# Kernel tuning notes

Hardware: AMD Instinct MI355X
Metric: run time of the kernel (lower is better)

Reference implementation:

```python
import jax, jax.numpy as jnp
import numpy as np

N, M = 100000, 800000
F_IN, F_E, H = 64, 16, 64
T_NODE, T_EDGE = 2, 3
HEAD_DIM = 16.0


def setup_inputs() -> dict:
    key = jax.random.key(0)
    ks = jax.random.split(key, 16)
    inp = {
        "x": jax.random.normal(ks[0], (N, F_IN), jnp.float32),
        "edge_feat": jax.random.normal(ks[1], (M, F_E), jnp.float32),
        "node_type": jax.random.randint(ks[2], (N,), 0, T_NODE, jnp.int32),
        "edge_src": jax.random.randint(ks[3], (M,), 0, N, jnp.int32),
        "edge_dst": jax.random.randint(ks[4], (M,), 0, N, jnp.int32),
        "edge_type": jax.random.randint(ks[5], (M,), 0, T_EDGE, jnp.int32),
    }
    s_n = 1.0 / np.sqrt(F_IN)
    s_e = 1.0 / np.sqrt(F_E)
    for i, name in enumerate(["W1", "W2", "W3", "W4"]):
        inp[name] = jax.random.normal(ks[6 + i], (T_NODE, F_IN, H), jnp.float32) * s_n
        inp["b" + name[1]] = jax.random.normal(ks[10 + i], (T_NODE, H), jnp.float32) * 0.01
    inp["W5"] = jax.random.normal(ks[14], (T_EDGE, F_E, H), jnp.float32) * s_e
    inp["b5"] = jax.random.normal(ks[15], (T_EDGE, H), jnp.float32) * 0.01
    return inp


def _node_proj(x, W, b, node_type):
    # per-node-type linear: [T,F,H] weights, select row per node type
    p = jnp.einsum('nf,tfh->tnh', x, W) + b[:, None, :]      # [T,N,H]
    return jnp.take_along_axis(p, node_type[None, :, None], axis=0)[0]  # [N,H]


def reference(x, edge_feat, W1, b1, W2, b2, W3, b3, W4, b4, W5, b5,
              node_type, edge_src, edge_dst, edge_type):
    n = x.shape[0]
    h1 = _node_proj(x, W1, b1, node_type)
    h2 = _node_proj(x, W2, b2, node_type)
    h3 = _node_proj(x, W3, b3, node_type)
    h4 = _node_proj(x, W4, b4, node_type)
    # per-edge-type linear via weight gather (F_E is small)
    w5e = jnp.einsum('mf,mfh->mh', edge_feat, W5[edge_type]) + b5[edge_type]  # [M,H]
    # scalar attention logit per edge (w3_i . (w4_j + w5_ij)) / sqrt(head_dim)
    num = jnp.sum(h3[edge_dst] * (h4[edge_src] + w5e), axis=-1)  # [M]
    # softmax over a single scalar per edge == 1.0 exactly (faithful to source)
    score = jax.nn.softmax((num / jnp.sqrt(HEAD_DIM))[:, None], axis=-1)[:, 0]  # [M]
    msg = score[:, None] * (h2[edge_src] + w5e)                  # [M,H]
    out = h1 + jax.ops.segment_sum(msg, edge_dst, num_segments=n)
    return out
```

## Files before the change

### kernel.cpp

```cpp
#include <hip/hip_runtime.h>


#define CAP 16
#define OVF_CAP 32768

typedef __attribute__((ext_vector_type(8))) short short8;
typedef __attribute__((ext_vector_type(4))) float f32x4;

__device__ __forceinline__ float b2f(unsigned short u) {
    union { unsigned v; float f; } x; x.v = ((unsigned)u) << 16; return x.f;
}
__device__ __forceinline__ unsigned short f2b(float f) {
    union { float f; unsigned v; } x; x.f = f;
    unsigned u = x.v;
    unsigned r = (u + 0x7FFFu + ((u >> 16) & 1u)) >> 16;
    return (unsigned short)r;
}

__global__ __launch_bounds__(256) void k1_gemm_scatter(
    const float* __restrict__ x, const int* __restrict__ nt,
    const float* __restrict__ W1, const float* __restrict__ b1,
    const float* __restrict__ W2, const float* __restrict__ b2,
    const int* __restrict__ esrc, const int* __restrict__ edst,
    const int* __restrict__ etype,
    int* __restrict__ cnt32, int* __restrict__ ovfCnt,
    int4* __restrict__ ovf, int2* __restrict__ rec,
    float* __restrict__ out, unsigned short* __restrict__ h2b,
    int N, int M)
{
    __shared__ __align__(16) unsigned short sx[128 * 72];
    __shared__ __align__(16) unsigned short sw[4][64 * 72];
    __shared__ int snt[128];

    int tid = threadIdx.x;

    if (blockIdx.x & 1) {
        int e0 = (blockIdx.x >> 1) * 1024 + tid;
        int dd[4], ssrc[4], tty[4];
        bool v[4];
#pragma unroll
        for (int j = 0; j < 4; ++j) {
            int e = e0 + j * 256;
            v[j] = e < M;
            int ec = v[j] ? e : 0;
            dd[j]   = edst[ec];
            ssrc[j] = esrc[ec];
            tty[j]  = etype[ec];
        }
        int pos[4];
#pragma unroll
        for (int j = 0; j < 4; ++j)
            if (v[j]) pos[j] = atomicAdd(&cnt32[dd[j]], 1);
#pragma unroll
        for (int j = 0; j < 4; ++j) {
            if (!v[j]) continue;
            int packed = ssrc[j] | (tty[j] << 20);
            int e = e0 + j * 256;
            if (pos[j] < CAP) {
                rec[dd[j] * CAP + pos[j]] = make_int2(packed, e);
            } else {
                int slot = atomicAdd(ovfCnt, 1);
                if (slot < OVF_CAP) ovf[slot] = make_int4(packed, e, dd[j], 0);
            }
        }
        return;
    }

    int rowbase = (blockIdx.x >> 1) * 128;

    const float* Wm0 = W1;
    const float* Wm1 = W1 + 4096;
    const float* Wm2 = W2;
    const float* Wm3 = W2 + 4096;
#pragma unroll
    for (int j = 0; j < 4; ++j) {
        int k  = (tid >> 4) + j * 16;
        int n4 = (tid & 15) * 4;
        float4 w0 = *(const float4*)&Wm0[k * 64 + n4];
        float4 w1v = *(const float4*)&Wm1[k * 64 + n4];
        float4 w2v = *(const float4*)&Wm2[k * 64 + n4];
        float4 w3 = *(const float4*)&Wm3[k * 64 + n4];
        sw[0][(n4 + 0) * 72 + k] = f2b(w0.x);
        sw[0][(n4 + 1) * 72 + k] = f2b(w0.y);
        sw[0][(n4 + 2) * 72 + k] = f2b(w0.z);
        sw[0][(n4 + 3) * 72 + k] = f2b(w0.w);
        sw[1][(n4 + 0) * 72 + k] = f2b(w1v.x);
        sw[1][(n4 + 1) * 72 + k] = f2b(w1v.y);
        sw[1][(n4 + 2) * 72 + k] = f2b(w1v.z);
        sw[1][(n4 + 3) * 72 + k] = f2b(w1v.w);
        sw[2][(n4 + 0) * 72 + k] = f2b(w2v.x);
        sw[2][(n4 + 1) * 72 + k] = f2b(w2v.y);
        sw[2][(n4 + 2) * 72 + k] = f2b(w2v.z);
        sw[2][(n4 + 3) * 72 + k] = f2b(w2v.w);
        sw[3][(n4 + 0) * 72 + k] = f2b(w3.x);
        sw[3][(n4 + 1) * 72 + k] = f2b(w3.y);
        sw[3][(n4 + 2) * 72 + k] = f2b(w3.z);
        sw[3][(n4 + 3) * 72 + k] = f2b(w3.w);
    }

    if (tid < 128) {
        int r = rowbase + tid;
        snt[tid] = (r < N) ? nt[r] : 0;
    }

    int fr = (tid & 15) * 4;
    int ir = tid >> 4;
#pragma unroll
    for (int it = 0; it < 8; ++it) {
        int i = it * 16 + ir;
        int r = rowbase + i;
        float4 v = make_float4(0.f, 0.f, 0.f, 0.f);
        if (r < N) v = *(const float4*)&x[(size_t)r * 64 + fr];
        ushort4 p;
        p.x = f2b(v.x); p.y = f2b(v.y); p.z = f2b(v.z); p.w = f2b(v.w);
        *(ushort4*)&sx[i * 72 + fr] = p;
    }
    __syncthreads();

    int lane = tid & 63;
    int wid  = tid >> 6;
    int q    = lane >> 4;
    int cc   = lane & 15;
    int m0   = wid * 32;

    f32x4 acc[4][2][4];
#pragma unroll
    for (int mm = 0; mm < 4; ++mm)
#pragma unroll
        for (int s = 0; s < 2; ++s)
#pragma unroll
            for (int t = 0; t < 4; ++t)
                acc[mm][s][t] = (f32x4){0.f, 0.f, 0.f, 0.f};

#pragma unroll
    for (int k0 = 0; k0 < 64; k0 += 32) {
        int ko = k0 + q * 8;
        short8 af0 = *(short8*)&sx[(m0 + cc) * 72 + ko];
        short8 af1 = *(short8*)&sx[(m0 + 16 + cc) * 72 + ko];
#pragma unroll
        for (int mm = 0; mm < 4; ++mm)
#pragma unroll
            for (int t = 0; t < 4; ++t) {
                short8 bf = *(short8*)&sw[mm][(t * 16 + cc) * 72 + ko];
                acc[mm][0][t] = __builtin_amdgcn_mfma_f32_16x16x32_bf16(
                    af0, bf, acc[mm][0][t], 0, 0, 0);
                acc[mm][1][t] = __builtin_amdgcn_mfma_f32_16x16x32_bf16(
                    af1, bf, acc[mm][1][t], 0, 0, 0);
            }
    }

    float b1v[2][4], b2v[2][4];
#pragma unroll
    for (int ty = 0; ty < 2; ++ty)
#pragma unroll
        for (int t = 0; t < 4; ++t) {
            b1v[ty][t] = b1[ty * 64 + t * 16 + cc];
            b2v[ty][t] = b2[ty * 64 + t * 16 + cc];
        }

#pragma unroll
    for (int s = 0; s < 2; ++s)
#pragma unroll
        for (int reg = 0; reg < 4; ++reg) {
            int rl = m0 + s * 16 + q * 4 + reg;
            int r = rowbase + rl;
            if (r < N) {
                int ty = snt[rl];
#pragma unroll
                for (int t = 0; t < 4; ++t) {
                    float v1 = (ty ? acc[1][s][t][reg] : acc[0][s][t][reg])
                               + b1v[ty][t];
                    float v2 = (ty ? acc[3][s][t][reg] : acc[2][s][t][reg])
                               + b2v[ty][t];
                    out[(size_t)r * 64 + t * 16 + cc] = v1;
                    h2b[(size_t)r * 64 + t * 16 + cc] = f2b(v2);
                }
            }
        }
}

__global__ __launch_bounds__(256) void k2_gather(
    const float* __restrict__ ef, const int2* __restrict__ rec,
    const int* __restrict__ cnt32,
    const float* __restrict__ W5, const float* __restrict__ b5,
    const int4* __restrict__ ovf, const int* __restrict__ ovfCnt,
    const unsigned short* __restrict__ h2b, float* __restrict__ out,
    int N, int gatherBlocks, int ovfBlocks)
{
    __shared__ float sW[3072 + 192];
    __shared__ float sG[4][64];

    int tid = threadIdx.x;
    for (int k = tid; k < 816; k += 256) {
        ((float4*)sW)[k] = (k < 768) ? ((const float4*)W5)[k]
                                     : ((const float4*)b5)[k - 768];
    }
    __syncthreads();

    int lane = tid & 63;
    int wid = tid >> 6;

    if (blockIdx.x >= (unsigned)gatherBlocks) {
        int novf = min(*ovfCnt, OVF_CAP);
        int gw = (blockIdx.x - gatherBlocks) * 4 + wid;
        int nw = ovfBlocks * 4;
        for (int ri = gw; ri < novf; ri += nw) {
            int4 o = ovf[ri];
            int s = o.x & 0xFFFFF;
            int t = (unsigned)o.x >> 20;
            float acc = sW[3072 + t * 64 + lane] +
                        b2f(h2b[(size_t)s * 64 + lane]);
#pragma unroll
            for (int f = 0; f < 16; ++f)
                acc = fmaf(ef[(size_t)o.y * 16 + f],
                           sW[(t * 16 + f) * 64 + lane], acc);
            unsafeAtomicAdd(&out[(size_t)o.z * 64 + lane], acc);
        }
        return;
    }

    int d = blockIdx.x * 4 + wid;
    bool active = d < N;
    int deg = 0;
    if (active) deg = min(cnt32[d], CAP);
    int base = d * CAP;

    int myt = (lane < 48) ? (lane >> 4) : (lane - 48);
    int myf = lane & 15;
    float accH = 0.f, accS = 0.f;

    for (int i = 0; i < deg; i += 8) {
        int nrem = deg - i;
        int2 r[8];
#pragma unroll
        for (int j = 0; j < 8; ++j) {
            int ij = i + j;
            ij = (ij < deg) ? ij : (deg - 1);
            r[j] = rec[base + ij];
        }
        float hv[8], ev[8];
#pragma unroll
        for (int j = 0; j < 8; ++j) {
            int s = r[j].x & 0xFFFFF;
            hv[j] = b2f(h2b[(size_t)s * 64 + lane]);
            ev[j] = ef[(size_t)r[j].y * 16 + myf];
        }
#pragma unroll
        for (int j = 0; j < 8; ++j) {
            int t = (unsigned)r[j].x >> 20;
            bool ok = j < nrem;
            accH += ok ? hv[j] : 0.f;
            float v = (lane < 48) ? ev[j] : 1.0f;
            accS += (ok && (t == myt)) ? v : 0.f;
        }
    }

    sG[wid][lane] = accS;
    float rr = accH;
    const float* g = sG[wid];
#pragma unroll
    for (int j = 0; j < 48; ++j)
        rr = fmaf(g[j], sW[j * 64 + lane], rr);
#pragma unroll
    for (int t = 0; t < 3; ++t)
        rr = fmaf(g[48 + t], sW[3072 + t * 64 + lane], rr);

    if (active)
        unsafeAtomicAdd(&out[(size_t)d * 64 + lane], rr);
}

extern "C" void kernel_launch(void* const* d_in, const int* in_sizes, int n_in,
                              void* d_out, int out_size, void* d_ws, size_t ws_size,
                              hipStream_t stream) {
    const float* x  = (const float*)d_in[0];
    const float* ef = (const float*)d_in[1];
    const int* nt   = (const int*)d_in[2];
    const int* es   = (const int*)d_in[3];
    const int* ed   = (const int*)d_in[4];
    const int* et   = (const int*)d_in[5];
    const float* W1 = (const float*)d_in[6];
    const float* b1 = (const float*)d_in[7];
    const float* W2 = (const float*)d_in[8];
    const float* b2 = (const float*)d_in[9];
    const float* W5 = (const float*)d_in[14];
    const float* b5 = (const float*)d_in[15];

    int N = in_sizes[2];
    int M = in_sizes[3];

    char* w = (char*)d_ws;
    size_t off = 0;
    unsigned short* h2b = (unsigned short*)(w + off); off += (size_t)N * 64 * 2;
    off = (off + 255) & ~(size_t)255;
    int2* rec = (int2*)(w + off); off += (size_t)N * CAP * 8;
    off = (off + 255) & ~(size_t)255;
    int4* ovf = (int4*)(w + off); off += (size_t)OVF_CAP * 16;
    off = (off + 255) & ~(size_t)255;
    int* ovfCnt = (int*)(w + off);
    int* cnt32  = (int*)(w + off + 64);
    size_t zeroBytes = 64 + (size_t)N * 4;

    float* out = (float*)d_out;

    hipMemsetAsync(ovfCnt, 0, zeroBytes, stream);

    int gemmBlocks    = (N + 127) / 128;
    int scatterBlocks = (M + 1023) / 1024;
    int gb1 = 2 * max(gemmBlocks, scatterBlocks);
    k1_gemm_scatter<<<gb1, 256, 0, stream>>>(
        x, nt, W1, b1, W2, b2, es, ed, et,
        cnt32, ovfCnt, ovf, rec, out, h2b, N, M);

    int gatherBlocks = (N + 3) / 4;
    int ovfBlocks = 32;
    k2_gather<<<gatherBlocks + ovfBlocks, 256, 0, stream>>>(
        ef, rec, cnt32, W5, b5, ovf, ovfCnt, h2b, out,
        N, gatherBlocks, ovfBlocks);
}
```

Measured before the change: 306.6 us.

## Replace capped per-node buckets with counting-sort binning by 32-node groups

```diff
diff --git a/kernel.cpp b/kernel.cpp
--- a/kernel.cpp
+++ b/kernel.cpp
@@ -1,8 +1,8 @@
 #include <hip/hip_runtime.h>
 
 
-#define CAP 16
-#define OVF_CAP 32768
+#define ABLK 64
+#define TS   3200
 
 typedef __attribute__((ext_vector_type(8))) short short8;
 typedef __attribute__((ext_vector_type(4))) float f32x4;
@@ -17,85 +17,121 @@
     return (unsigned short)r;
 }
 
-__global__ __launch_bounds__(256) void k1_gemm_scatter(
+__global__ __launch_bounds__(256) void k_hist(
+    const int* __restrict__ edst, int* __restrict__ table,
+    int M, int NB, int epb)
+{
+    __shared__ int h[TS];
+    int tid = threadIdx.x;
+    for (int t = tid; t < TS; t += 256) h[t] = 0;
+    __syncthreads();
+    int base = blockIdx.x * epb;
+    for (int i = tid; i < epb; i += 256) {
+        int e = base + i;
+        if (e < M) atomicAdd(&h[edst[e] >> 5], 1);
+    }
+    __syncthreads();
+    for (int t = tid; t < NB; t += 256) table[blockIdx.x * TS + t] = h[t];
+}
+
+__global__ __launch_bounds__(256) void k_colsum(
+    const int* __restrict__ table, int* __restrict__ totals, int NB)
+{
+    int t = blockIdx.x * 256 + threadIdx.x;
+    if (t >= NB) return;
+    int s = 0;
+    for (int j = 0; j < ABLK; ++j) s += table[j * TS + t];
+    totals[t] = s;
+}
+
+__global__ __launch_bounds__(256) void k_prefix(
+    const int* __restrict__ totals, int* __restrict__ starts, int NB, int M)
+{
+    __shared__ int ps[256];
+    int tid = threadIdx.x;
+    int per = (NB + 255) / 256;
+    int lo = tid * per, hi = min(lo + per, NB);
+    int s = 0;
+    for (int i = lo; i < hi; ++i) s += totals[i];
+    ps[tid] = s;
+    __syncthreads();
+    int run = s;
+    for (int off = 1; off < 256; off <<= 1) {
+        int tmp = (tid >= off) ? ps[tid - off] : 0;
+        __syncthreads();
+        run += tmp;
+        ps[tid] = run;
+        __syncthreads();
+    }
+    int r = run - s;
+    for (int i = lo; i < hi; ++i) { starts[i] = r; r += totals[i]; }
+    if (tid == 255) starts[NB] = M;
+}
+
+__global__ __launch_bounds__(256) void k_offsets(
+    int* __restrict__ table, const int* __restrict__ starts, int NB)
+{
+    int t = blockIdx.x * 256 + threadIdx.x;
+    if (t >= NB) return;
+    int run = starts[t];
+    for (int j = 0; j < ABLK; ++j) {
+        int v = table[j * TS + t];
+        table[j * TS + t] = run;
+        run += v;
+    }
+}
+
+__global__ __launch_bounds__(256) void k3_gemm_binscatter(
     const float* __restrict__ x, const int* __restrict__ nt,
     const float* __restrict__ W1, const float* __restrict__ b1,
     const float* __restrict__ W2, const float* __restrict__ b2,
     const int* __restrict__ esrc, const int* __restrict__ edst,
     const int* __restrict__ etype,
-    int* __restrict__ cnt32, int* __restrict__ ovfCnt,
-    int4* __restrict__ ovf, int2* __restrict__ rec,
+    const int* __restrict__ table, int2* __restrict__ rec,
     float* __restrict__ out, unsigned short* __restrict__ h2b,
-    int N, int M)
-{
-    __shared__ __align__(16) unsigned short sx[128 * 72];
-    __shared__ __align__(16) unsigned short sw[4][64 * 72];
-    __shared__ int snt[128];
+    int N, int M, int NB, int epb)
+{
+    __shared__ __align__(16) char smem[55808];
 
     int tid = threadIdx.x;
 
-    if (blockIdx.x & 1) {
-        int e0 = (blockIdx.x >> 1) * 1024 + tid;
-        int dd[4], ssrc[4], tty[4];
-        bool v[4];
-#pragma unroll
-        for (int j = 0; j < 4; ++j) {
-            int e = e0 + j * 256;
-            v[j] = e < M;
-            int ec = v[j] ? e : 0;
-            dd[j]   = edst[ec];
-            ssrc[j] = esrc[ec];
-            tty[j]  = etype[ec];
-        }
-        int pos[4];
-#pragma unroll
-        for (int j = 0; j < 4; ++j)
-            if (v[j]) pos[j] = atomicAdd(&cnt32[dd[j]], 1);
-#pragma unroll
-        for (int j = 0; j < 4; ++j) {
-            if (!v[j]) continue;
-            int packed = ssrc[j] | (tty[j] << 20);
-            int e = e0 + j * 256;
-            if (pos[j] < CAP) {
-                rec[dd[j] * CAP + pos[j]] = make_int2(packed, e);
-            } else {
-                int slot = atomicAdd(ovfCnt, 1);
-                if (slot < OVF_CAP) ovf[slot] = make_int4(packed, e, dd[j], 0);
-            }
+    if (blockIdx.x < ABLK) {
+        int* loc = (int*)smem;
+        int b = blockIdx.x;
+        for (int t = tid; t < NB; t += 256) loc[t] = table[b * TS + t];
+        __syncthreads();
+        int base = b * epb;
+        for (int i = tid; i < epb; i += 256) {
+            int e = base + i;
+            if (e >= M) break;
+            int d = edst[e];
+            int bkt = d >> 5, dloc = d & 31;
+            int pos = atomicAdd(&loc[bkt], 1);
+            int packed = esrc[e] | (etype[e] << 17) | (dloc << 19);
+            rec[pos] = make_int2(packed, e);
         }
         return;
     }
 
-    int rowbase = (blockIdx.x >> 1) * 128;
-
-    const float* Wm0 = W1;
-    const float* Wm1 = W1 + 4096;
-    const float* Wm2 = W2;
-    const float* Wm3 = W2 + 4096;
+    unsigned short* sx = (unsigned short*)smem;
+    unsigned short* sw = (unsigned short*)(smem + 18432);
+    int* snt = (int*)(smem + 55296);
+
+    int rowbase = (blockIdx.x - ABLK) * 128;
+
+    const float* Wm[4] = { W1, W1 + 4096, W2, W2 + 4096 };
 #pragma unroll
     for (int j = 0; j < 4; ++j) {
         int k  = (tid >> 4) + j * 16;
         int n4 = (tid & 15) * 4;
-        float4 w0 = *(const float4*)&Wm0[k * 64 + n4];
-        float4 w1v = *(const float4*)&Wm1[k * 64 + n4];
-        float4 w2v = *(const float4*)&Wm2[k * 64 + n4];
-        float4 w3 = *(const float4*)&Wm3[k * 64 + n4];
-        sw[0][(n4 + 0) * 72 + k] = f2b(w0.x);
-        sw[0][(n4 + 1) * 72 + k] = f2b(w0.y);
-        sw[0][(n4 + 2) * 72 + k] = f2b(w0.z);
-        sw[0][(n4 + 3) * 72 + k] = f2b(w0.w);
-        sw[1][(n4 + 0) * 72 + k] = f2b(w1v.x);
-        sw[1][(n4 + 1) * 72 + k] = f2b(w1v.y);
-        sw[1][(n4 + 2) * 72 + k] = f2b(w1v.z);
-        sw[1][(n4 + 3) * 72 + k] = f2b(w1v.w);
-        sw[2][(n4 + 0) * 72 + k] = f2b(w2v.x);
-        sw[2][(n4 + 1) * 72 + k] = f2b(w2v.y);
-        sw[2][(n4 + 2) * 72 + k] = f2b(w2v.z);
-        sw[2][(n4 + 3) * 72 + k] = f2b(w2v.w);
-        sw[3][(n4 + 0) * 72 + k] = f2b(w3.x);
-        sw[3][(n4 + 1) * 72 + k] = f2b(w3.y);
-        sw[3][(n4 + 2) * 72 + k] = f2b(w3.z);
-        sw[3][(n4 + 3) * 72 + k] = f2b(w3.w);
+#pragma unroll
+        for (int mm = 0; mm < 4; ++mm) {
+            float4 wv = *(const float4*)&Wm[mm][k * 64 + n4];
+            sw[mm * 4608 + (n4 + 0) * 72 + k] = f2b(wv.x);
+            sw[mm * 4608 + (n4 + 1) * 72 + k] = f2b(wv.y);
+            sw[mm * 4608 + (n4 + 2) * 72 + k] = f2b(wv.z);
+            sw[mm * 4608 + (n4 + 3) * 72 + k] = f2b(wv.w);
+        }
     }
 
     if (tid < 128) {
@@ -141,7 +177,7 @@
         for (int mm = 0; mm < 4; ++mm)
 #pragma unroll
             for (int t = 0; t < 4; ++t) {
-                short8 bf = *(short8*)&sw[mm][(t * 16 + cc) * 72 + ko];
+                short8 bf = *(short8*)&sw[mm * 4608 + (t * 16 + cc) * 72 + ko];
                 acc[mm][0][t] = __builtin_amdgcn_mfma_f32_16x16x32_bf16(
                     af0, bf, acc[mm][0][t], 0, 0, 0);
                 acc[mm][1][t] = __builtin_amdgcn_mfma_f32_16x16x32_bf16(
@@ -179,94 +215,79 @@
         }
 }
 
-__global__ __launch_bounds__(256) void k2_gather(
+__global__ __launch_bounds__(256) void k4_gather(
     const float* __restrict__ ef, const int2* __restrict__ rec,
-    const int* __restrict__ cnt32,
+    const int* __restrict__ starts,
     const float* __restrict__ W5, const float* __restrict__ b5,
-    const int4* __restrict__ ovf, const int* __restrict__ ovfCnt,
-    const unsigned short* __restrict__ h2b, float* __restrict__ out,
-    int N, int gatherBlocks, int ovfBlocks)
-{
-    __shared__ float sW[3072 + 192];
-    __shared__ float sG[4][64];
+    const unsigned short* __restrict__ h2b, float* __restrict__ out, int N)
+{
+    __shared__ float sW[3264];
+    __shared__ float sH[32 * 64];
+    __shared__ float sS[32 * 52];
 
     int tid = threadIdx.x;
-    for (int k = tid; k < 816; k += 256) {
+    for (int k = tid; k < 816; k += 256)
         ((float4*)sW)[k] = (k < 768) ? ((const float4*)W5)[k]
                                      : ((const float4*)b5)[k - 768];
-    }
-    __syncthreads();
+    for (int k = tid; k < 2048; k += 256) sH[k] = 0.f;
+    for (int k = tid; k < 1664; k += 256) sS[k] = 0.f;
+    __syncthreads();
+
+    int b = blockIdx.x;
+    int beg = starts[b];
+    int nE = starts[b + 1] - beg;
 
     int lane = tid & 63;
-    int wid = tid >> 6;
-
-    if (blockIdx.x >= (unsigned)gatherBlocks) {
-        int novf = min(*ovfCnt, OVF_CAP);
-        int gw = (blockIdx.x - gatherBlocks) * 4 + wid;
-        int nw = ovfBlocks * 4;
-        for (int ri = gw; ri < novf; ri += nw) {
-            int4 o = ovf[ri];
-            int s = o.x & 0xFFFFF;
-            int t = (unsigned)o.x >> 20;
-            float acc = sW[3072 + t * 64 + lane] +
-                        b2f(h2b[(size_t)s * 64 + lane]);
-#pragma unroll
-            for (int f = 0; f < 16; ++f)
-                acc = fmaf(ef[(size_t)o.y * 16 + f],
-                           sW[(t * 16 + f) * 64 + lane], acc);
-            unsafeAtomicAdd(&out[(size_t)o.z * 64 + lane], acc);
-        }
-        return;
-    }
-
-    int d = blockIdx.x * 4 + wid;
-    bool active = d < N;
-    int deg = 0;
-    if (active) deg = min(cnt32[d], CAP);
-    int base = d * CAP;
-
+    int wid  = tid >> 6;
+    int qq = (nE + 3) >> 2;
+    int lo = wid * qq, hi = min(lo + qq, nE);
+
+    int myf = lane & 15;
+    bool sLane = lane < 51;
     int myt = (lane < 48) ? (lane >> 4) : (lane - 48);
-    int myf = lane & 15;
-    float accH = 0.f, accS = 0.f;
-
-    for (int i = 0; i < deg; i += 8) {
-        int nrem = deg - i;
+
+    for (int i = lo; i < hi; i += 8) {
+        int nrem = hi - i;
         int2 r[8];
 #pragma unroll
         for (int j = 0; j < 8; ++j) {
             int ij = i + j;
-            ij = (ij < deg) ? ij : (deg - 1);
-            r[j] = rec[base + ij];
+            ij = (ij < hi) ? ij : (hi - 1);
+            r[j] = rec[beg + ij];
         }
         float hv[8], ev[8];
 #pragma unroll
         for (int j = 0; j < 8; ++j) {
-            int s = r[j].x & 0xFFFFF;
+            int s = r[j].x & 0x1FFFF;
             hv[j] = b2f(h2b[(size_t)s * 64 + lane]);
             ev[j] = ef[(size_t)r[j].y * 16 + myf];
         }
 #pragma unroll
         for (int j = 0; j < 8; ++j) {
-            int t = (unsigned)r[j].x >> 20;
             bool ok = j < nrem;
-            accH += ok ? hv[j] : 0.f;
-            float v = (lane < 48) ? ev[j] : 1.0f;
-            accS += (ok && (t == myt)) ? v : 0.f;
-        }
-    }
-
-    sG[wid][lane] = accS;
-    float rr = accH;
-    const float* g = sG[wid];
-#pragma unroll
-    for (int j = 0; j < 48; ++j)
-        rr = fmaf(g[j], sW[j * 64 + lane], rr);
-#pragma unroll
-    for (int t = 0; t < 3; ++t)
-        rr = fmaf(g[48 + t], sW[3072 + t * 64 + lane], rr);
-
-    if (active)
-        unsafeAtomicAdd(&out[(size_t)d * 64 + lane], rr);
+            int t  = (r[j].x >> 17) & 3;
+            int dl = (r[j].x >> 19) & 31;
+            if (ok) {
+                atomicAdd(&sH[dl * 64 + lane], hv[j]);
+                float v = (lane < 48) ? ev[j] : 1.0f;
+                if (sLane && t == myt) atomicAdd(&sS[dl * 52 + lane], v);
+            }
+        }
+    }
+    __syncthreads();
+
+    for (int dl = wid * 8; dl < wid * 8 + 8; ++dl) {
+        int d = b * 32 + dl;
+        if (d >= N) break;
+        float rr = sH[dl * 64 + lane];
+#pragma unroll
+        for (int j = 0; j < 48; ++j)
+            rr = fmaf(sS[dl * 52 + j], sW[j * 64 + lane], rr);
+#pragma unroll
+        for (int t = 0; t < 3; ++t)
+            rr = fmaf(sS[dl * 52 + 48 + t], sW[3072 + t * 64 + lane], rr);
+        out[(size_t)d * 64 + lane] += rr;
+    }
 }
 
 extern "C" void kernel_launch(void* const* d_in, const int* in_sizes, int n_in,
@@ -287,33 +308,32 @@
 
     int N = in_sizes[2];
     int M = in_sizes[3];
+    int NB = (N + 31) >> 5;
+    int epb = (M + ABLK - 1) / ABLK;
 
     char* w = (char*)d_ws;
     size_t off = 0;
     unsigned short* h2b = (unsigned short*)(w + off); off += (size_t)N * 64 * 2;
     off = (off + 255) & ~(size_t)255;
-    int2* rec = (int2*)(w + off); off += (size_t)N * CAP * 8;
+    int2* rec   = (int2*)(w + off); off += (size_t)M * 8;
     off = (off + 255) & ~(size_t)255;
-    int4* ovf = (int4*)(w + off); off += (size_t)OVF_CAP * 16;
-    off = (off + 255) & ~(size_t)255;
-    int* ovfCnt = (int*)(w + off);
-    int* cnt32  = (int*)(w + off + 64);
-    size_t zeroBytes = 64 + (size_t)N * 4;
+    int* table  = (int*)(w + off);  off += (size_t)ABLK * TS * 4;
+    int* totals = (int*)(w + off);  off += (size_t)(NB + 64) * 4;
+    int* starts = (int*)(w + off);  off += (size_t)(NB + 64) * 4;
 
     float* out = (float*)d_out;
 
-    hipMemsetAsync(ovfCnt, 0, zeroBytes, stream);
-
-    int gemmBlocks    = (N + 127) / 128;
-    int scatterBlocks = (M + 1023) / 1024;
-    int gb1 = 2 * max(gemmBlocks, scatterBlocks);
-    k1_gemm_scatter<<<gb1, 256, 0, stream>>>(
-        x, nt, W1, b1, W2, b2, es, ed, et,
-        cnt32, ovfCnt, ovf, rec, out, h2b, N, M);
-
-    int gatherBlocks = (N + 3) / 4;
-    int ovfBlocks = 32;
-    k2_gather<<<gatherBlocks + ovfBlocks, 256, 0, stream>>>(
-        ef, rec, cnt32, W5, b5, ovf, ovfCnt, h2b, out,
-        N, gatherBlocks, ovfBlocks);
-}
+    k_hist<<<ABLK, 256, 0, stream>>>(ed, table, M, NB, epb);
+
+    int cb = (NB + 255) / 256;
+    k_colsum<<<cb, 256, 0, stream>>>(table, totals, NB);
+    k_prefix<<<1, 256, 0, stream>>>(totals, starts, NB, M);
+    k_offsets<<<cb, 256, 0, stream>>>(table, starts, NB);
+
+    int gemmBlocks = (N + 127) / 128;
+    k3_gemm_binscatter<<<ABLK + gemmBlocks, 256, 0, stream>>>(
+        x, nt, W1, b1, W2, b2, es, ed, et, table, rec, out, h2b,
+        N, M, NB, epb);
+
+    k4_gather<<<NB, 256, 0, stream>>>(ef, rec, starts, W5, b5, h2b, out, N);
+}
```

After: 593.9 us. +93.7%, slower.
